# Optimization experiments

Hardware: AMD Instinct MI355X
Metric: run time of the kernel (lower is better)

## Reference

```python
import jax, jax.numpy as jnp
import numpy as np

SIM_THRESHOLD = 0.95
NUM_SAMPLES = 2048
EPS_NORM = 1e-12  # F.normalize eps
EPS_DENOM = 1e-6


def setup_inputs() -> dict:
    key = jax.random.key(0)
    k1, k2, k3 = jax.random.split(key, 3)
    B, K, C, H, W = 2, 8, 256, 128, 128
    masks_logits = jax.random.normal(k1, (B, K, H, W), dtype=jnp.float32)
    upsampler_features = jax.random.normal(k2, (B, C, H, W), dtype=jnp.float32)
    # per-batch randperm[:S], mirroring torch.randperm(H*W)[:S]
    perm_keys = jax.random.split(k3, B)
    indices = jnp.stack([
        jax.random.permutation(pk, H * W)[:NUM_SAMPLES] for pk in perm_keys
    ]).astype(jnp.int32)  # (B, S)
    return {"masks_logits": masks_logits,
            "upsampler_features": upsampler_features,
            "indices": indices}


def reference(masks_logits, upsampler_features, indices):
    B, K, H, W = masks_logits.shape
    C = upsampler_features.shape[1]
    probs = jax.nn.sigmoid(masks_logits).reshape(B, K, H * W)
    feats = upsampler_features.reshape(B, C, H * W)
    idx = indices[:, None, :]  # (B,1,S)
    f_sample = jnp.take_along_axis(feats, idx, axis=2)          # (B,C,S)
    norm = jnp.linalg.norm(f_sample, axis=1, keepdims=True)
    f_sample = f_sample / jnp.maximum(norm, EPS_NORM)
    m_sample = jnp.take_along_axis(probs, idx, axis=2)          # (B,K,S)
    sim = jnp.einsum('bcs,bct->bst', f_sample, f_sample)        # (B,S,S)
    pos = (sim > SIM_THRESHOLD).astype(jnp.float32)             # (B,S,S)
    m_diff = jnp.abs(m_sample[:, :, :, None] - m_sample[:, :, None, :])  # (B,K,S,S)
    num = jnp.sum(m_diff * pos[:, None, :, :])
    den = jnp.sum(pos) + EPS_DENOM
    return num / den
```

## Files before the change

kernel.cpp:

```cpp
#include <hip/hip_runtime.h>
#include <hip/hip_bf16.h>
#include <math.h>

#define Bn 2
#define Kn 8
#define Cn 256
#define HWn (128*128)
#define Sn 2048
#define BT 128
#define BK 64
#define NSTEP (Cn / BK)
#define SIM_BLOCKS ((Sn/BT)*(Sn/BT)*Bn)

typedef __bf16 bf16x8 __attribute__((ext_vector_type(8)));
typedef float  f32x4  __attribute__((ext_vector_type(4)));

__device__ __forceinline__ void gload_lds16(const ushort* g, ushort* l) {
    __builtin_amdgcn_global_load_lds(
        (const __attribute__((address_space(1))) void*)g,
        (__attribute__((address_space(3))) void*)l,
        16, 0, 0);
}

__device__ __forceinline__ float bf16_to_f32(ushort u) {
    union { unsigned int i; float f; } cv;
    cv.i = ((unsigned int)u) << 16;
    return cv.f;
}

__global__ __launch_bounds__(256) void transpose_kernel(
    const float* __restrict__ feats, ushort* __restrict__ featsT)
{
    __shared__ float lds[64][65];
    const int b  = blockIdx.z;
    const int C0 = blockIdx.y * 64;
    const int H0 = blockIdx.x * 64;
    const int t  = threadIdx.x;

    const float* base = feats + ((size_t)(b * Cn + C0)) * HWn + H0;
    const int c_l = t >> 4;
    const int h4  = (t & 15) * 4;
    #pragma unroll
    for (int i = 0; i < 4; ++i) {
        const float4 v = *reinterpret_cast<const float4*>(
            base + (size_t)(c_l + 16 * i) * HWn + h4);
        lds[h4 + 0][c_l + 16 * i] = v.x;
        lds[h4 + 1][c_l + 16 * i] = v.y;
        lds[h4 + 2][c_l + 16 * i] = v.z;
        lds[h4 + 3][c_l + 16 * i] = v.w;
    }
    __syncthreads();
    const int h  = t >> 2;
    const int c0 = (t & 3) * 16;
    ushort u[16];
    #pragma unroll
    for (int e = 0; e < 16; ++e) {
        __hip_bfloat16 hv = __float2bfloat16(lds[h][c0 + e]);
        u[e] = *reinterpret_cast<const ushort*>(&hv);
    }
    ushort* dst = featsT + ((size_t)(b * HWn + H0 + h)) * Cn + C0 + c0;
    *reinterpret_cast<uint4*>(dst)     = *reinterpret_cast<const uint4*>(&u[0]);
    *reinterpret_cast<uint4*>(dst + 8) = *reinterpret_cast<const uint4*>(&u[8]);
}

__global__ __launch_bounds__(256) void gather2_kernel(
    const float* __restrict__ masks, const ushort* __restrict__ featsT,
    const int* __restrict__ indices, ushort* __restrict__ fTb,
    float* __restrict__ mS)
{
    const int wave = threadIdx.x >> 6;
    const int lane = threadIdx.x & 63;
    const int bs = blockIdx.x * 4 + wave;
    const int b  = bs >> 11;
    const int s  = bs & (Sn - 1);
    const int id = indices[b * Sn + s];

    const ushort4 raw = *reinterpret_cast<const ushort4*>(
        featsT + ((size_t)(b * HWn + id)) * Cn + lane * 4);
    float v[4] = { bf16_to_f32(raw.x), bf16_to_f32(raw.y),
                   bf16_to_f32(raw.z), bf16_to_f32(raw.w) };

    float x = v[0]*v[0] + v[1]*v[1] + v[2]*v[2] + v[3]*v[3];
    #pragma unroll
    for (int o = 32; o > 0; o >>= 1) x += __shfl_xor(x, o);
    const float scale = 1.0f / fmaxf(sqrtf(x), 1e-12f);

    ushort o4[4];
    #pragma unroll
    for (int q = 0; q < 4; ++q) {
        __hip_bfloat16 hv = __float2bfloat16(v[q] * scale);
        o4[q] = *reinterpret_cast<const ushort*>(&hv);
    }
    *reinterpret_cast<ushort4*>(fTb + (size_t)bs * Cn + lane * 4) =
        *reinterpret_cast<const ushort4*>(&o4[0]);

    if (lane < Kn) {
        const float lg = masks[((size_t)(b * Kn + lane)) * HWn + id];
        mS[(size_t)bs * Kn + lane] = 1.0f / (1.0f + expf(-lg));
    }
}

__global__ __launch_bounds__(256) void gather_kernel(
    const float* __restrict__ masks, const float* __restrict__ feats,
    const int* __restrict__ indices, ushort* __restrict__ fTb,
    float* __restrict__ mS)
{
    const int wave = threadIdx.x >> 6;
    const int lane = threadIdx.x & 63;
    const int bs = blockIdx.x * 4 + wave;
    const int b  = bs >> 11;
    const int s  = bs & (Sn - 1);
    const int id = indices[b * Sn + s];

    const float* fb = feats + (size_t)b * Cn * HWn + id;
    float v[4];
    #pragma unroll
    for (int q = 0; q < 4; ++q)
        v[q] = fb[(size_t)(lane + 64 * q) * HWn];

    float x = v[0]*v[0] + v[1]*v[1] + v[2]*v[2] + v[3]*v[3];
    #pragma unroll
    for (int o = 32; o > 0; o >>= 1) x += __shfl_xor(x, o);
    const float scale = 1.0f / fmaxf(sqrtf(x), 1e-12f);

    #pragma unroll
    for (int q = 0; q < 4; ++q) {
        __hip_bfloat16 hv = __float2bfloat16(v[q] * scale);
        fTb[(size_t)bs * Cn + lane + 64 * q] = *reinterpret_cast<const ushort*>(&hv);
    }

    if (lane < Kn) {
        const float lg = masks[((size_t)(b * Kn + lane)) * HWn + id];
        mS[(size_t)bs * Kn + lane] = 1.0f / (1.0f + expf(-lg));
    }
}

__global__ __launch_bounds__(512, 4) void sim_kernel(
    const ushort* __restrict__ fTb, const float* __restrict__ mS,
    float* __restrict__ part)
{
    __shared__ ushort ldsA[2][BT * BK];
    __shared__ ushort ldsB[2][BT * BK];

    const int b   = blockIdx.z;
    const int s0  = blockIdx.y * BT;
    const int t0  = blockIdx.x * BT;
    const int tid = threadIdx.x;
    const int lane = tid & 63;
    const int wave = tid >> 6;
    const int wm = wave >> 2;
    const int wn = wave & 3;
    const int l15 = lane & 15, l4 = lane >> 4;

    const ushort* FA = fTb + ((size_t)(b * Sn + s0)) * Cn;
    const ushort* FB = fTb + ((size_t)(b * Sn + t0)) * Cn;

    #define STAGE(buf, k0)                                                     \
    {                                                                          \
        _Pragma("unroll")                                                      \
        for (int i = 0; i < 2; ++i) {                                          \
            const int q   = tid + i * 512;                                     \
            const int row = q >> 3;                                            \
            const int csw = (q & 7) ^ (row & 7);                               \
            const size_t goff = (size_t)row * Cn + (k0) + csw * 8;             \
            gload_lds16(FA + goff, &ldsA[buf][q * 8]);                         \
            gload_lds16(FB + goff, &ldsB[buf][q * 8]);                         \
        }                                                                      \
    }

    f32x4 acc[4][2];
    #pragma unroll
    for (int m = 0; m < 4; ++m)
        #pragma unroll
        for (int n = 0; n < 2; ++n) acc[m][n] = (f32x4){0.f, 0.f, 0.f, 0.f};

    STAGE(0, 0);
    __syncthreads();

    #pragma unroll
    for (int s = 0; s < NSTEP; ++s) {
        const int buf = s & 1;
        if (s + 1 < NSTEP) STAGE(buf ^ 1, (s + 1) * BK);

        #pragma unroll
        for (int kk = 0; kk < BK; kk += 32) {
            const int g = (kk >> 3) + l4;
            bf16x8 aF[4], bF[2];
            #pragma unroll
            for (int m = 0; m < 4; ++m) {
                const int row = wm * 64 + m * 16 + l15;
                aF[m] = *reinterpret_cast<const bf16x8*>(
                    &ldsA[buf][row * BK + ((g ^ (row & 7)) << 3)]);
            }
            #pragma unroll
            for (int n = 0; n < 2; ++n) {
                const int row = wn * 32 + n * 16 + l15;
                bF[n] = *reinterpret_cast<const bf16x8*>(
                    &ldsB[buf][row * BK + ((g ^ (row & 7)) << 3)]);
            }
            #pragma unroll
            for (int m = 0; m < 4; ++m)
                #pragma unroll
                for (int n = 0; n < 2; ++n)
                    acc[m][n] = __builtin_amdgcn_mfma_f32_16x16x32_bf16(
                        aF[m], bF[n], acc[m][n], 0, 0, 0);
        }
        __syncthreads();
    }

    float num_l = 0.0f, den_l = 0.0f;
    const float* mSb = mS + (size_t)b * Sn * Kn;
    #pragma unroll
    for (int m = 0; m < 4; ++m) {
        #pragma unroll
        for (int n = 0; n < 2; ++n) {
            #pragma unroll
            for (int r = 0; r < 4; ++r) {
                if (acc[m][n][r] > 0.95f) {
                    den_l += 1.0f;
                    const int srow = s0 + wm * 64 + m * 16 + l4 * 4 + r;
                    const int tcol = t0 + wn * 32 + n * 16 + l15;
                    const float* ma = mSb + (size_t)srow * Kn;
                    const float* mb = mSb + (size_t)tcol * Kn;
                    #pragma unroll
                    for (int k = 0; k < Kn; ++k) num_l += fabsf(ma[k] - mb[k]);
                }
            }
        }
    }

    #pragma unroll
    for (int o = 32; o > 0; o >>= 1) {
        num_l += __shfl_down(num_l, o);
        den_l += __shfl_down(den_l, o);
    }
    __shared__ float rn[8], rd[8];
    if (lane == 0) { rn[wave] = num_l; rd[wave] = den_l; }
    __syncthreads();
    if (tid == 0) {
        float nn = 0.f, dd = 0.f;
        #pragma unroll
        for (int w = 0; w < 8; ++w) { nn += rn[w]; dd += rd[w]; }
        const int bid = (blockIdx.z * gridDim.y + blockIdx.y) * gridDim.x + blockIdx.x;
        part[2 * bid]     = nn;
        part[2 * bid + 1] = dd;
    }
}

__global__ __launch_bounds__(256) void finalize_kernel(
    const float* __restrict__ part, float* __restrict__ out)
{
    const int tid = threadIdx.x;
    float n = 0.f, d = 0.f;
    #pragma unroll
    for (int i = 0; i < SIM_BLOCKS / 256; ++i) {
        const float2 p = reinterpret_cast<const float2*>(part)[tid + 256 * i];
        n += p.x; d += p.y;
    }
    #pragma unroll
    for (int o = 32; o > 0; o >>= 1) {
        n += __shfl_down(n, o);
        d += __shfl_down(d, o);
    }
    __shared__ float sn[4], sd[4];
    if ((tid & 63) == 0) { sn[tid >> 6] = n; sd[tid >> 6] = d; }
    __syncthreads();
    if (tid == 0) {
        const float fn = sn[0] + sn[1] + sn[2] + sn[3];
        const float fd = sd[0] + sd[1] + sd[2] + sd[3];
        out[0] = fn / (fd + 1e-6f);
    }
}

extern "C" void kernel_launch(void* const* d_in, const int* in_sizes, int n_in,
                              void* d_out, int out_size, void* d_ws, size_t ws_size,
                              hipStream_t stream) {
    const float* masks   = (const float*)d_in[0];
    const float* feats   = (const float*)d_in[1];
    const int*   indices = (const int*)d_in[2];
    float* out = (float*)d_out;

    const size_t fTb_b   = (size_t)Bn * Sn * Cn * sizeof(ushort);
    const size_t mS_b    = (size_t)Bn * Sn * Kn * sizeof(float);
    const size_t part_b  = (size_t)SIM_BLOCKS * 2 * sizeof(float);
    const size_t featsT_b = (size_t)Bn * HWn * Cn * sizeof(ushort);

    ushort* fTb   = (ushort*)d_ws;
    float*  mSm   = (float*)((char*)d_ws + fTb_b);
    float*  part  = (float*)((char*)d_ws + fTb_b + mS_b);
    ushort* featsT = (ushort*)((char*)d_ws + fTb_b + mS_b + part_b);

    if (ws_size >= fTb_b + mS_b + part_b + featsT_b) {
        dim3 tg(HWn / 64, Cn / 64, Bn);
        transpose_kernel<<<tg, 256, 0, stream>>>(feats, featsT);
        gather2_kernel<<<Bn * Sn / 4, 256, 0, stream>>>(masks, featsT, indices, fTb, mSm);
    } else {
        gather_kernel<<<Bn * Sn / 4, 256, 0, stream>>>(masks, feats, indices, fTb, mSm);
    }
    dim3 grid(Sn / BT, Sn / BT, Bn);
    sim_kernel<<<grid, 512, 0, stream>>>(fTb, mSm, part);
    finalize_kernel<<<1, 256, 0, stream>>>(part, out);
}
```

Baseline: 29.13 us.

## Replace double-buffered BK=64 pipeline with single-buffered two-stage BK=128 loads

The sim kernel now loads 128-wide channel slabs into a single LDS buffer per operand and runs two stages, where it used to prefetch four 64-wide stages into double buffers. The XOR swizzle widens from 8 to 16 groups to match the larger row. This cuts the number of barriers and stages, but it gives up the overlap between global loads and MFMA work. LDS use per block stays the same.

```diff
diff --git a/kernel.cpp b/kernel.cpp
--- a/kernel.cpp
+++ b/kernel.cpp
@@ -8,8 +8,8 @@
 #define HWn (128*128)
 #define Sn 2048
 #define BT 128
-#define BK 64
-#define NSTEP (Cn / BK)
+#define BKc 128
+#define NSTAGE (Cn / BKc)
 #define SIM_BLOCKS ((Sn/BT)*(Sn/BT)*Bn)
 
 typedef __bf16 bf16x8 __attribute__((ext_vector_type(8)));
@@ -139,8 +139,8 @@
     const ushort* __restrict__ fTb, const float* __restrict__ mS,
     float* __restrict__ part)
 {
-    __shared__ ushort ldsA[2][BT * BK];
-    __shared__ ushort ldsB[2][BT * BK];
+    __shared__ ushort ldsA[BT * BKc];
+    __shared__ ushort ldsB[BT * BKc];
 
     const int b   = blockIdx.z;
     const int s0  = blockIdx.y * BT;
@@ -155,48 +155,41 @@
     const ushort* FA = fTb + ((size_t)(b * Sn + s0)) * Cn;
     const ushort* FB = fTb + ((size_t)(b * Sn + t0)) * Cn;
 
-    #define STAGE(buf, k0)                                                     \
-    {                                                                          \
-        _Pragma("unroll")                                                      \
-        for (int i = 0; i < 2; ++i) {                                          \
-            const int q   = tid + i * 512;                                     \
-            const int row = q >> 3;                                            \
-            const int csw = (q & 7) ^ (row & 7);                               \
-            const size_t goff = (size_t)row * Cn + (k0) + csw * 8;             \
-            gload_lds16(FA + goff, &ldsA[buf][q * 8]);                         \
-            gload_lds16(FB + goff, &ldsB[buf][q * 8]);                         \
-        }                                                                      \
-    }
-
     f32x4 acc[4][2];
     #pragma unroll
     for (int m = 0; m < 4; ++m)
         #pragma unroll
         for (int n = 0; n < 2; ++n) acc[m][n] = (f32x4){0.f, 0.f, 0.f, 0.f};
 
-    STAGE(0, 0);
-    __syncthreads();
-
-    #pragma unroll
-    for (int s = 0; s < NSTEP; ++s) {
-        const int buf = s & 1;
-        if (s + 1 < NSTEP) STAGE(buf ^ 1, (s + 1) * BK);
-
-        #pragma unroll
-        for (int kk = 0; kk < BK; kk += 32) {
+    #pragma unroll
+    for (int st = 0; st < NSTAGE; ++st) {
+        const int k0 = st * BKc;
+        #pragma unroll
+        for (int i = 0; i < 4; ++i) {
+            const int q   = tid + i * 512;
+            const int row = q >> 4;
+            const int csw = (q & 15) ^ (row & 15);
+            const size_t goff = (size_t)row * Cn + k0 + csw * 8;
+            gload_lds16(FA + goff, &ldsA[q * 8]);
+            gload_lds16(FB + goff, &ldsB[q * 8]);
+        }
+        __syncthreads();
+
+        #pragma unroll
+        for (int kk = 0; kk < BKc; kk += 32) {
             const int g = (kk >> 3) + l4;
             bf16x8 aF[4], bF[2];
             #pragma unroll
             for (int m = 0; m < 4; ++m) {
                 const int row = wm * 64 + m * 16 + l15;
                 aF[m] = *reinterpret_cast<const bf16x8*>(
-                    &ldsA[buf][row * BK + ((g ^ (row & 7)) << 3)]);
+                    &ldsA[row * BKc + ((g ^ (row & 15)) << 3)]);
             }
             #pragma unroll
             for (int n = 0; n < 2; ++n) {
                 const int row = wn * 32 + n * 16 + l15;
                 bF[n] = *reinterpret_cast<const bf16x8*>(
-                    &ldsB[buf][row * BK + ((g ^ (row & 7)) << 3)]);
+                    &ldsB[row * BKc + ((g ^ (row & 15)) << 3)]);
             }
             #pragma unroll
             for (int m = 0; m < 4; ++m)
```

Result: faster. 28.15 us (-3.4%).
